# Optimization experiments

Hardware: AMD Instinct MI355X
Metric: run time of the kernel (lower is better)

The kernel has to match this reference:

```python
import jax, jax.numpy as jnp
import numpy as np
import math

A = 32; B = 32; PSIZE = 16; K = 3; STRIDE = 2; PAD = 1; ITERS = 3; FINAL_LAMBDA = 0.01
KK = K * K; KKA = KK * A; KKA2 = KKA // 2 + 1
EPS = 1e-12; LN2PI = math.log(2 * math.pi)


def unfold(x, k, s, p):
    # torch F.unfold: output feature dim ordered (C, kh, kw), columns row-major
    b, C, h, w = x.shape
    xp = jnp.pad(x, ((0, 0), (0, 0), (p, p), (p, p)))
    oh = (h + 2 * p - k) // s + 1
    ow = (w + 2 * p - k) // s + 1
    cols = [xp[:, :, ki:ki + s * (oh - 1) + 1:s, kj:kj + s * (ow - 1) + 1:s]
            for ki in range(k) for kj in range(k)]
    patches = jnp.stack(cols, axis=2)  # [b, C, kk, oh, ow]
    return patches.reshape(b, C, k * k, oh * ow), oh, ow


def setup_inputs():
    key = jax.random.key(0)
    ks = jax.random.split(key, 8)
    b, h, w = 4, 14, 14
    a_in = jax.random.uniform(ks[0], (b, A, h, w), dtype=jnp.float32)
    pose = jax.random.normal(ks[1], (b, A * PSIZE, h, w), dtype=jnp.float32)
    mpose_w = jax.random.normal(ks[2], (B * PSIZE, PSIZE), dtype=jnp.float32) / np.float32(np.sqrt(PSIZE))
    mpose_b = jnp.zeros((B * PSIZE,), jnp.float32)
    freq_w = jax.random.normal(ks[3], (KKA2, PSIZE, 2), dtype=jnp.float32) * 0.02
    ln_g = jnp.ones((A,), jnp.float32)
    ln_b = jnp.zeros((A,), jnp.float32)
    lim = np.float32(np.sqrt(6.0 / (KK + KK)))  # xavier_uniform on [kk, kk, 1]
    spat_w = jax.random.uniform(ks[4], (KK, KK, 1), jnp.float32, -lim, lim)
    spat_bias = jnp.ones((KK,), jnp.float32)
    beta_u = jnp.zeros((1, 1, B, 1), jnp.float32)
    beta_a = jnp.zeros((1, 1, B), jnp.float32)
    return dict(a_in=a_in, pose=pose, mpose_w=mpose_w, mpose_b=mpose_b,
                freq_w=freq_w, ln_g=ln_g, ln_b=ln_b, spat_w=spat_w,
                spat_bias=spat_bias, beta_u=beta_u, beta_a=beta_a)


def _forward(a_in, pose, mpose_w, mpose_b, freq_w, ln_g, ln_b,
             spat_w, spat_bias, beta_u, beta_a):
    b = a_in.shape[0]
    pose_u, oh, ow = unfold(pose, K, STRIDE, PAD)  # [b, A*PSIZE, KK, l]
    l = oh * ow
    pose_u = pose_u.reshape(b, A, PSIZE, KK, l)
    pose_u = pose_u.transpose(0, 4, 3, 1, 2).reshape(b, l, KKA, PSIZE)
    # mpose linear: psize -> B*psize
    po = jnp.einsum('blkp,qp->blkq', pose_u, mpose_w) + mpose_b
    po = po.reshape(b * l, KKA, B, PSIZE)
    # Frequency FFT filter over kkA axis (weight shared across all B slices)
    xf = jnp.fft.rfft(po, axis=1, norm='ortho')        # [bl, KKA2, B, PSIZE] complex
    wc = freq_w[..., 0] + 1j * freq_w[..., 1]           # [KKA2, PSIZE]
    xf = xf * wc[None, :, None, :]
    po = jnp.fft.irfft(xf, n=KKA, axis=1, norm='ortho') + po  # residual
    v = po.reshape(b, l, KKA, B, PSIZE)
    a_u, _, _ = unfold(a_in, K, STRIDE, PAD)            # [b, A, KK, l]
    a_u = a_u.transpose(0, 3, 2, 1).reshape(b, l, KKA)
    # Spatial gating applied to ones-initialized r (identical for every B slice)
    ones = jnp.ones((b * l, KKA), jnp.float32)
    g = ones.reshape(b * l, KK, A)
    mu_g = g.mean(-1, keepdims=True)
    var_g = ((g - mu_g) ** 2).mean(-1, keepdims=True)
    gn = (g - mu_g) / jnp.sqrt(var_g + 1e-5) * ln_g + ln_b
    g2 = jnp.einsum('ij,nja->nia', spat_w[:, :, 0], gn) + spat_bias[None, :, None]
    gate = jax.nn.gelu(g2, approximate=False).reshape(b * l, KKA) + ones
    logit = jnp.broadcast_to(gate[:, :, None], (b * l, KKA, B))
    r = jax.nn.softmax(logit, axis=2).reshape(b, l, KKA, B, 1)
    a_out = mu = None
    for i in range(ITERS):
        lam = FINAL_LAMBDA * (1.0 - 0.95 ** (i + 1))
        # m-step
        rr = r * a_u[:, :, :, None, None]
        r_sum = rr.sum(axis=2, keepdims=True)                 # [b,l,1,B,1]
        coeff = rr / (r_sum + EPS)
        mu = (coeff * v).sum(axis=2, keepdims=True)           # [b,l,1,B,PSIZE]
        sig = (coeff * (v - mu) ** 2).sum(axis=2, keepdims=True) + EPS
        cost = (beta_u + jnp.log(jnp.sqrt(sig[:, :, 0]))) * r_sum[:, :, 0]  # [b,l,B,PSIZE]
        a_out = jax.nn.sigmoid(lam * (beta_a - cost.sum(axis=3)))           # [b,l,B]
        if i < ITERS - 1:
            # e-step (note: log(sigma_sq * ln2pi) is faithful to the original code)
            ln_p = (-0.5 * jnp.sum(jnp.log(sig * LN2PI), axis=-1)
                    - jnp.sum((v - mu) ** 2 / (2.0 * sig), axis=-1))        # [b,l,KKA,B]
            ln_ap = ln_p + jnp.log(a_out[:, :, None, :])
            r = jax.nn.softmax(ln_ap, axis=-1)[..., None]
    pose_out = mu[:, :, 0].reshape(b, l, B * PSIZE).transpose(0, 2, 1).reshape(b, B * PSIZE, oh, ow)
    a_fin = a_out.transpose(0, 2, 1).reshape(b, B, oh, ow)
    return a_fin, pose_out


def reference(a_in, pose, mpose_w, mpose_b, freq_w, ln_g, ln_b,
              spat_w, spat_bias, beta_u, beta_a):
    return _forward(a_in, pose, mpose_w, mpose_b, freq_w, ln_g, ln_b,
                    spat_w, spat_bias, beta_u, beta_a)
```

## Files before the change

kernel.cpp:

```cpp
#include <hip/hip_runtime.h>
#include <hip/hip_bf16.h>
#include <math.h>

#define A_    32
#define B_    32
#define PS    16
#define KK_   9
#define KKA_  288
#define OH_   7
#define L_    49
#define NB    4
#define NSITE 196

#define LAM1 5.0e-4f
#define LAM2 9.75e-4f
#define LAM3 1.42625e-3f
#define LOG_LN2PI 0.6086775903077413f

typedef _Float16 half2v __attribute__((ext_vector_type(2)));
typedef _Float16 half4v __attribute__((ext_vector_type(4)));
typedef short    short8 __attribute__((ext_vector_type(8)));
typedef float    floatx4 __attribute__((ext_vector_type(4)));

#if defined(__has_attribute)
#  if __has_attribute(amdgpu_num_vgpr)
#    define KEM_VGPR_ATTR __attribute__((amdgpu_num_vgpr(224)))
#  else
#    define KEM_VGPR_ATTR
#  endif
#else
#  define KEM_VGPR_ATTR
#endif

static __device__ __forceinline__ float san(float x, float lo, float hi){
    return fminf(fmaxf(x, lo), hi);
}

static __device__ __forceinline__ float dot2acc(half2v a, half2v b, float c){
#if __has_builtin(__builtin_amdgcn_fdot2)
    return __builtin_amdgcn_fdot2(a, b, c, false);
#else
    return c + (float)a.x*(float)b.x + (float)a.y*(float)b.y;
#endif
}

static __device__ __forceinline__ void sched_fence(){
#if __has_builtin(__builtin_amdgcn_sched_barrier)
    __builtin_amdgcn_sched_barrier(0);
#else
    asm volatile("" ::: "memory");
#endif
}

__global__ void k_prep(const float* __restrict__ fw, const float* __restrict__ pose,
                       ushort* __restrict__ cpr, float* __restrict__ csum,
                       __hip_bfloat16* __restrict__ Xt, int n0, int cols, int nx)
{
    if ((int)blockIdx.x >= nx){
        int id = ((int)blockIdx.x - nx)*256 + threadIdx.x;
        if (id >= 16*288) return;
        int p = id / 288, m = id % 288;
        float acc = fw[(0*16 + p)*2 + 0];
        for (int k = 1; k <= 143; ++k){
            float re = fw[(k*16 + p)*2 + 0];
            float im = fw[(k*16 + p)*2 + 1];
            int km = (k*m) % 288;
            float ang = 0.021816615649929116f * (float)km;
            float s, c; sincosf(ang, &s, &c);
            acc += 2.0f*(re*c - im*s);
        }
        float re144 = fw[(144*16 + p)*2 + 0];
        acc += re144 * ((m & 1) ? -1.0f : 1.0f);
        float cv = acc * (1.0f/288.0f);
        if (m == 0) cv += 1.0f;
        cv = san(cv, -1e4f, 1e4f);

        __hip_bfloat16 hb = __float2bfloat16(cv);
        float hif = __bfloat162float(hb);
        __hip_bfloat16 lb = __float2bfloat16(cv - hif);
        ushort hi = *(ushort*)&hb, lo = *(ushort*)&lb;

        ushort* c0h = cpr + p*592;
        ushort* c1h = cpr + 16*592   + p*592;
        ushort* c0l = cpr + 16*592*2 + p*592;
        ushort* c1l = cpr + 16*592*3 + p*592;
        int x1 = 288 - m;
        c0h[x1] = hi;  c0l[x1] = lo;
        c1h[x1-1] = hi; c1l[x1-1] = lo;
        if (m >= 1){
            int x2 = 576 - m;
            c0h[x2] = hi;  c0l[x2] = lo;
            c1h[x2-1] = hi; c1l[x2-1] = lo;
        } else {
            c0h[0] = hi; c0l[0] = lo;
            csum[p] = san(1.0f + fw[(0*16 + p)*2 + 0], -1e4f, 1e4f);
        }
        return;
    }
    int id = blockIdx.x*256 + threadIdx.x;
    if (id >= cols*KKA_) return;
    int c = id / KKA_, j = id % KKA_;
    int n = n0 + (c >> 4), q = c & 15;
    int bs = n / L_, l = n % L_, oy = l / OH_, ox = l % OH_;
    int kk = j >> 5, a = j & 31;
    int y = oy*2 - 1 + kk/3, x = ox*2 - 1 + kk%3;
    float v = 0.f;
    if ((unsigned)y < 14u && (unsigned)x < 14u)
        v = pose[((bs*(A_*PS) + a*PS + q)*14 + y)*14 + x];
    Xt[id] = __float2bfloat16(san(v, -1e4f, 1e4f));
}

__launch_bounds__(256)
__global__ void k_stageB(const ushort* __restrict__ cpr, const __hip_bfloat16* __restrict__ Xt,
                         _Float16* __restrict__ U, int cols, int ns)
{
    const int bx = blockIdx.x, by = blockIdx.y, p = blockIdx.z;
    const int t = threadIdx.x;
    const int w = t >> 6, lane = t & 63;
    const int mn = lane & 15, quad = lane >> 4;
    const int i0 = by*48;
    const int col = bx*64 + w*16 + mn;
    const int colc = (col < cols) ? col : (cols - 1);

    const ushort* c0h = cpr + p*592;
    const ushort* c1h = cpr + 16*592   + p*592;
    const ushort* c0l = cpr + 16*592*2 + p*592;
    const ushort* c1l = cpr + 16*592*3 + p*592;

    floatx4 acc[3] = {{0,0,0,0},{0,0,0,0},{0,0,0,0}};
    for (int k0 = 0; k0 < 288; k0 += 32){
        short8 bfrag = *(const short8*)&Xt[colc*KKA_ + k0 + quad*8];
        #pragma unroll
        for (int s = 0; s < 3; ++s){
            int o = 288 + k0 + quad*8 - (i0 + s*16 + mn);
            int sel = o & 1;
            int off = o - sel;
            const ushort* bh = sel ? c1h : c0h;
            const ushort* bl = sel ? c1l : c0l;
            short8 ah = *(const short8*)&bh[off];
            short8 al = *(const short8*)&bl[off];
            acc[s] = __builtin_amdgcn_mfma_f32_16x16x32_bf16(ah, bfrag, acc[s], 0, 0, 0);
            acc[s] = __builtin_amdgcn_mfma_f32_16x16x32_bf16(al, bfrag, acc[s], 0, 0, 0);
        }
    }
    if (col < cols){
        const int nn = col >> 4, q0 = col & 15;
        #pragma unroll
        for (int s = 0; s < 3; ++s){
            #pragma unroll
            for (int r = 0; r < 4; ++r){
                int i = i0 + s*16 + quad*4 + r;
                U[(i*ns + nn)*256 + p*16 + q0] = (_Float16)acc[s][r];
            }
        }
    }
}

__launch_bounds__(512, 2) KEM_VGPR_ATTR
__global__ void
k_em(const _Float16* __restrict__ U, const float* __restrict__ a_in,
     const float* __restrict__ mpw, const float* __restrict__ mpb,
     const float* __restrict__ csum,
     const float* __restrict__ beta_u, const float* __restrict__ beta_a,
     int n0, int ns, float* __restrict__ out)
{
    const int nl = blockIdx.x;
    const int n  = n0 + nl;
    const int t = threadIdx.x;
    const int Bc = t >> 4, p = t & 15;
    const int bs = n / L_, l = n % L_;

    __shared__ uint  v_lds[72][512];
    __shared__ float a_s[KKA_];
    __shared__ float d_s[16][33];
    __shared__ float rbuf[16][33];
    __shared__ float cst[32];

    for (int j = t; j < KKA_; j += 512){
        int kk = j >> 5, a = j & 31;
        int oy = l / OH_, ox = l % OH_;
        int y = oy*2 - 1 + kk/3, x = ox*2 - 1 + kk%3;
        float v = 0.f;
        if ((unsigned)y < 14u && (unsigned)x < 14u)
            v = a_in[((bs*A_ + a)*14 + y)*14 + x];
        a_s[j] = san(v, 0.f, 1e4f);
    }
    half2v w_h[8];
    #pragma unroll
    for (int k = 0; k < 8; ++k){
        w_h[k].x = (_Float16)mpw[t*16 + 2*k];
        w_h[k].y = (_Float16)mpw[t*16 + 2*k + 1];
    }
    const float vb = mpb[t] * csum[p];
    const float bu = beta_u[Bc];
    const float ba = beta_a[Bc];
    __syncthreads();

    float S0tot = 0.f;
    for (int j = 0; j < KKA_; ++j) S0tot += a_s[j];

    const _Float16* Up = U + nl*256 + p*16;
    const int istr = ns*256;

    float S1 = 0.f, S2 = 0.f;

    half2v v_h[72];
    #pragma unroll
    for (int g = 0; g < 36; ++g){
        #pragma unroll
        for (int k2 = 0; k2 < 2; ++k2){
            const int pr = g*2 + k2;
            const int i0 = 144 + pr*2;
            union { uint4 u4; half2v h2[4]; } A0, A1, B0, B1;
            A0.u4 = *(const uint4*)&Up[i0*istr];
            A1.u4 = *(const uint4*)&Up[i0*istr + 8];
            B0.u4 = *(const uint4*)&Up[(i0+1)*istr];
            B1.u4 = *(const uint4*)&Up[(i0+1)*istr + 8];
            float v0 = vb, v1 = vb;
            #pragma unroll
            for (int m = 0; m < 4; ++m){
                v0 = dot2acc(A0.h2[m], w_h[m],   v0);
                v0 = dot2acc(A1.h2[m], w_h[4+m], v0);
                v1 = dot2acc(B0.h2[m], w_h[m],   v1);
                v1 = dot2acc(B1.h2[m], w_h[4+m], v1);
            }
            const float a0 = a_s[i0], a1 = a_s[i0+1];
            S1 += a0*v0 + a1*v1;
            S2 += a0*v0*v0 + a1*v1*v1;
            half2v vh; vh.x = (_Float16)v0; vh.y = (_Float16)v1;
            v_h[pr] = vh;
        }
        sched_fence();
    }

    for (int ch = 0; ch < 9; ++ch){
        #pragma unroll
        for (int k = 0; k < 8; ++k){
            const int i0 = ch*16 + 2*k;
            union { uint4 u4; half2v h2[4]; } A0, A1, B0, B1;
            A0.u4 = *(const uint4*)&Up[i0*istr];
            A1.u4 = *(const uint4*)&Up[i0*istr + 8];
            B0.u4 = *(const uint4*)&Up[(i0+1)*istr];
            B1.u4 = *(const uint4*)&Up[(i0+1)*istr + 8];
            float v0 = vb, v1 = vb;
            #pragma unroll
            for (int m = 0; m < 4; ++m){
                v0 = dot2acc(A0.h2[m], w_h[m],   v0);
                v0 = dot2acc(A1.h2[m], w_h[4+m], v0);
                v1 = dot2acc(B0.h2[m], w_h[m],   v1);
                v1 = dot2acc(B1.h2[m], w_h[4+m], v1);
            }
            const float a0 = a_s[i0], a1 = a_s[i0+1];
            S1 += a0*v0 + a1*v1;
            S2 += a0*v0*v0 + a1*v1*v1;
            union { half2v h; uint u; } cv;
            cv.h.x = (_Float16)v0; cv.h.y = (_Float16)v1;
            v_lds[ch*8 + k][t] = cv.u;
        }
    }

    float mu_r, i2s_r;
    {
        const float rs  = S0tot * (1.0f/32.0f);
        const float inv = 1.0f / (rs + 1e-12f);
        const float S1r = S1 * (1.0f/32.0f), S2r = S2 * (1.0f/32.0f);
        mu_r = S1r * inv;
        const float sg  = fmaxf((S2r - 2.f*mu_r*S1r + mu_r*mu_r*rs) * inv, 0.f) + 1e-12f;
        i2s_r = 0.5f / sg;
        const float lg  = logf(sg);
        float cs = (bu + 0.5f*lg) * rs;
        float ls = lg + LOG_LN2PI;
        #pragma unroll
        for (int m = 1; m < 16; m <<= 1){ cs += __shfl_xor(cs, m, 16); ls += __shfl_xor(ls, m, 16); }
        const float aout = san(1.f/(1.f + expf(-LAM1*(ba - cs))), 1e-30f, 1.f);
        if (p == 0) cst[Bc] = logf(aout) - 0.5f*ls;
    }
    __syncthreads();

    const int b0 = p & 1, b1 = (p>>1)&1, b2 = (p>>2)&1, b3 = (p>>3)&1;
    float muF = 0.f, aF = 0.f;
    for (int it = 0; it < 2; ++it){
        const float lam = it ? LAM3 : LAM2;
        float T0 = 0.f, T1 = 0.f, T2 = 0.f;

        auto process = [&](int ibase, auto getpair){
            float e1[8], e2[4], e3[2], dfin;
            #pragma unroll
            for (int s = 0; s < 8; ++s){
                float v0, v1; getpair(s, v0, v1);
                float d0 = v0 - mu_r, d1 = v1 - mu_r;
                float ea = d0*d0*i2s_r, eb = d1*d1*i2s_r;
                float aown  = b0 ? eb : ea;
                float asend = b0 ? ea : eb;
                e1[s] = aown + __shfl_xor(asend, 1);
            }
            #pragma unroll
            for (int s = 0; s < 4; ++s){
                float aown  = b1 ? e1[2*s+1] : e1[2*s];
                float asend = b1 ? e1[2*s]   : e1[2*s+1];
                e2[s] = aown + __shfl_xor(asend, 2);
            }
            #pragma unroll
            for (int s = 0; s < 2; ++s){
                float aown  = b2 ? e2[2*s+1] : e2[2*s];
                float asend = b2 ? e2[2*s]   : e2[2*s+1];
                e3[s] = aown + __shfl_xor(asend, 4);
            }
            {
                float aown  = b3 ? e3[1] : e3[0];
                float asend = b3 ? e3[0] : e3[1];
                dfin = aown + __shfl_xor(asend, 8);
            }
            d_s[p][Bc] = dfin;
            __syncthreads();
            {
                const int isub = t >> 5, Bce = t & 31;
                float lnap = cst[Bce] - d_s[isub][Bce];
                float mx = lnap;
                #pragma unroll
                for (int m = 16; m >= 1; m >>= 1) mx = fmaxf(mx, __shfl_xor(mx, m));
                float ex = expf(lnap - mx);
                float sm = ex;
                #pragma unroll
                for (int m = 16; m >= 1; m >>= 1) sm += __shfl_xor(sm, m);
                rbuf[isub][Bce] = (ex / sm) * a_s[ibase + isub];
            }
            __syncthreads();
            #pragma unroll
            for (int s = 0; s < 8; ++s){
                float v0, v1; getpair(s, v0, v1);
                float r0 = rbuf[2*s][Bc], r1 = rbuf[2*s+1][Bc];
                T0 += r0 + r1;
                T1 += r0*v0 + r1*v1;
                T2 += r0*v0*v0 + r1*v1*v1;
            }
        };

        for (int ch = 0; ch < 9; ++ch){
            process(ch*16, [&](int s, float& v0, float& v1){
                union { uint u; half2v h; } cv; cv.u = v_lds[ch*8 + s][t];
                v0 = (float)cv.h.x; v1 = (float)cv.h.y;
            });
        }
        #pragma unroll
        for (int ch = 0; ch < 9; ++ch){
            process(144 + ch*16, [&](int s, float& v0, float& v1){
                half2v vh = v_h[ch*8 + s];
                v0 = (float)vh.x; v1 = (float)vh.y;
            });
        }

        const float inv = 1.f/(T0 + 1e-12f);
        const float mu  = T1 * inv;
        const float sg  = fmaxf((T2 - 2.f*mu*T1 + mu*mu*T0) * inv, 0.f) + 1e-12f;
        const float lg  = logf(sg);
        float cs = (bu + 0.5f*lg) * T0;
        float ls = lg + LOG_LN2PI;
        #pragma unroll
        for (int m = 1; m < 16; m <<= 1){ cs += __shfl_xor(cs, m, 16); ls += __shfl_xor(ls, m, 16); }
        const float aout = san(1.f/(1.f + expf(-lam*(ba - cs))), 1e-30f, 1.f);
        if (it == 0){
            mu_r = mu; i2s_r = 0.5f/sg;
            if (p == 0) cst[Bc] = logf(aout) - 0.5f*ls;
            __syncthreads();
        } else { muF = mu; aF = aout; }
    }

    if (p == 0) out[bs*(B_*L_) + Bc*L_ + l] = san(aF, 0.f, 1.f);
    out[6272 + (bs*512 + t)*L_ + l] = san(muF, -1e4f, 1e4f);
}

extern "C" void kernel_launch(void* const* d_in, const int* in_sizes, int n_in,
                              void* d_out, int out_size, void* d_ws, size_t ws_size,
                              hipStream_t stream)
{
    const float* a_in   = (const float*)d_in[0];
    const float* pose   = (const float*)d_in[1];
    const float* mpw    = (const float*)d_in[2];
    const float* mpb    = (const float*)d_in[3];
    const float* fw     = (const float*)d_in[4];
    const float* beta_u = (const float*)d_in[9];
    const float* beta_a = (const float*)d_in[10];
    float* out = (float*)d_out;

    char* base = (char*)d_ws;
    float*  csum = (float*)(base + 0);
    ushort* cpr  = (ushort*)(base + 256);

    const int opts[] = {196, 98, 49, 28, 14, 7, 4, 2, 1};
    int ns = 1;
    for (int oi = 0; oi < 9; ++oi){
        size_t need = 76288u + (size_t)156672u * (size_t)opts[oi];
        if (need <= ws_size){ ns = opts[oi]; break; }
    }
    const int G = NSITE / ns;
    const int cols = ns * PS;
    __hip_bfloat16* Xt = (__hip_bfloat16*)(base + 76288);
    _Float16*       Ug = (_Float16*)(base + 76288 + (size_t)9216*ns);

    for (int g = 0; g < G; ++g){
        const int n0 = g * ns;
        const int nx = (cols*KKA_ + 255)/256;
        const int nc = (g == 0) ? 18 : 0;
        k_prep  <<<nx + nc, 256, 0, stream>>>(fw, pose, cpr, csum, Xt, n0, cols, nx);
        k_stageB<<<dim3((cols + 63)/64, 6, 16), 256, 0, stream>>>(cpr, Xt, Ug, cols, ns);
        k_em    <<<ns, 512, 0, stream>>>(Ug, a_in, mpw, mpb, csum, beta_u, beta_a, n0, ns, out);
    }
}
```

Before: 281.1 us.

## Batch three E-step chunks per barrier pair and reorder prep blocks

The E-step loop in k_em now handles 48 input capsules (three 16-row groups) between each pair of __syncthreads, instead of 16, which cuts barrier count threefold. The separate rbuf array is merged into an enlarged d_s buffer that holds the responsibilities in place. k_prep now schedules the coefficient-table blocks first so the long sincos loops start early, and uses the fast __sincosf intrinsic. The cost is more registers and LDS per step, plus slightly lower sincos accuracy.

Measured after the change: 258.2 us. 1.09x faster.

```diff
diff --git a/kernel.cpp b/kernel.cpp
--- a/kernel.cpp
+++ b/kernel.cpp
@@ -54,10 +54,10 @@
 
 __global__ void k_prep(const float* __restrict__ fw, const float* __restrict__ pose,
                        ushort* __restrict__ cpr, float* __restrict__ csum,
-                       __hip_bfloat16* __restrict__ Xt, int n0, int cols, int nx)
+                       __hip_bfloat16* __restrict__ Xt, int n0, int cols, int nc)
 {
-    if ((int)blockIdx.x >= nx){
-        int id = ((int)blockIdx.x - nx)*256 + threadIdx.x;
+    if ((int)blockIdx.x < nc){
+        int id = (int)blockIdx.x*256 + threadIdx.x;
         if (id >= 16*288) return;
         int p = id / 288, m = id % 288;
         float acc = fw[(0*16 + p)*2 + 0];
@@ -66,7 +66,7 @@
             float im = fw[(k*16 + p)*2 + 1];
             int km = (k*m) % 288;
             float ang = 0.021816615649929116f * (float)km;
-            float s, c; sincosf(ang, &s, &c);
+            float s, c; __sincosf(ang, &s, &c);
             acc += 2.0f*(re*c - im*s);
         }
         float re144 = fw[(144*16 + p)*2 + 0];
@@ -97,7 +97,7 @@
         }
         return;
     }
-    int id = blockIdx.x*256 + threadIdx.x;
+    int id = ((int)blockIdx.x - nc)*256 + threadIdx.x;
     if (id >= cols*KKA_) return;
     int c = id / KKA_, j = id % KKA_;
     int n = n0 + (c >> 4), q = c & 15;
@@ -171,9 +171,8 @@
     const int bs = n / L_, l = n % L_;
 
     __shared__ uint  v_lds[72][512];
+    __shared__ float d_s[48][33];
     __shared__ float a_s[KKA_];
-    __shared__ float d_s[16][33];
-    __shared__ float rbuf[16][33];
     __shared__ float cst[32];
 
     for (int j = t; j < KKA_; j += 512){
@@ -283,73 +282,82 @@
         const float lam = it ? LAM3 : LAM2;
         float T0 = 0.f, T1 = 0.f, T2 = 0.f;
 
-        auto process = [&](int ibase, auto getpair){
-            float e1[8], e2[4], e3[2], dfin;
+        #pragma unroll
+        for (int ch = 0; ch < 6; ++ch){
             #pragma unroll
-            for (int s = 0; s < 8; ++s){
-                float v0, v1; getpair(s, v0, v1);
-                float d0 = v0 - mu_r, d1 = v1 - mu_r;
-                float ea = d0*d0*i2s_r, eb = d1*d1*i2s_r;
-                float aown  = b0 ? eb : ea;
-                float asend = b0 ? ea : eb;
-                e1[s] = aown + __shfl_xor(asend, 1);
-            }
-            #pragma unroll
-            for (int s = 0; s < 4; ++s){
-                float aown  = b1 ? e1[2*s+1] : e1[2*s];
-                float asend = b1 ? e1[2*s]   : e1[2*s+1];
-                e2[s] = aown + __shfl_xor(asend, 2);
-            }
-            #pragma unroll
-            for (int s = 0; s < 2; ++s){
-                float aown  = b2 ? e2[2*s+1] : e2[2*s];
-                float asend = b2 ? e2[2*s]   : e2[2*s+1];
-                e3[s] = aown + __shfl_xor(asend, 4);
-            }
-            {
-                float aown  = b3 ? e3[1] : e3[0];
-                float asend = b3 ? e3[0] : e3[1];
-                dfin = aown + __shfl_xor(asend, 8);
-            }
-            d_s[p][Bc] = dfin;
+            for (int g = 0; g < 3; ++g){
+                float e1[8], e2[4], e3[2], dfin;
+                #pragma unroll
+                for (int s = 0; s < 8; ++s){
+                    const int pr = ch*24 + g*8 + s;
+                    float v0, v1;
+                    if (ch < 3){
+                        union { uint u; half2v h; } cv; cv.u = v_lds[pr][t];
+                        v0 = (float)cv.h.x; v1 = (float)cv.h.y;
+                    } else {
+                        half2v vh = v_h[pr - 72];
+                        v0 = (float)vh.x; v1 = (float)vh.y;
+                    }
+                    float d0 = v0 - mu_r, d1 = v1 - mu_r;
+                    float ea = d0*d0*i2s_r, eb = d1*d1*i2s_r;
+                    float aown  = b0 ? eb : ea;
+                    float asend = b0 ? ea : eb;
+                    e1[s] = aown + __shfl_xor(asend, 1);
+                }
+                #pragma unroll
+                for (int s = 0; s < 4; ++s){
+                    float aown  = b1 ? e1[2*s+1] : e1[2*s];
+                    float asend = b1 ? e1[2*s]   : e1[2*s+1];
+                    e2[s] = aown + __shfl_xor(asend, 2);
+                }
+                #pragma unroll
+                for (int s = 0; s < 2; ++s){
+                    float aown  = b2 ? e2[2*s+1] : e2[2*s];
+                    float asend = b2 ? e2[2*s]   : e2[2*s+1];
+                    e3[s] = aown + __shfl_xor(asend, 4);
+                }
+                {
+                    float aown  = b3 ? e3[1] : e3[0];
+                    float asend = b3 ? e3[0] : e3[1];
+                    dfin = aown + __shfl_xor(asend, 8);
+                }
+                d_s[g*16 + p][Bc] = dfin;
+            }
             __syncthreads();
             {
                 const int isub = t >> 5, Bce = t & 31;
-                float lnap = cst[Bce] - d_s[isub][Bce];
-                float mx = lnap;
                 #pragma unroll
-                for (int m = 16; m >= 1; m >>= 1) mx = fmaxf(mx, __shfl_xor(mx, m));
-                float ex = expf(lnap - mx);
-                float sm = ex;
-                #pragma unroll
-                for (int m = 16; m >= 1; m >>= 1) sm += __shfl_xor(sm, m);
-                rbuf[isub][Bce] = (ex / sm) * a_s[ibase + isub];
+                for (int rr = 0; rr < 3; ++rr){
+                    const int row = rr*16 + isub;
+                    float lnap = cst[Bce] - d_s[row][Bce];
+                    float mx = lnap;
+                    #pragma unroll
+                    for (int m = 16; m >= 1; m >>= 1) mx = fmaxf(mx, __shfl_xor(mx, m));
+                    float ex = expf(lnap - mx);
+                    float sm = ex;
+                    #pragma unroll
+                    for (int m = 16; m >= 1; m >>= 1) sm += __shfl_xor(sm, m);
+                    d_s[row][Bce] = (ex / sm) * a_s[ch*48 + row];
+                }
             }
             __syncthreads();
             #pragma unroll
-            for (int s = 0; s < 8; ++s){
-                float v0, v1; getpair(s, v0, v1);
-                float r0 = rbuf[2*s][Bc], r1 = rbuf[2*s+1][Bc];
+            for (int s = 0; s < 24; ++s){
+                const int pr = ch*24 + s;
+                float v0, v1;
+                if (ch < 3){
+                    union { uint u; half2v h; } cv; cv.u = v_lds[pr][t];
+                    v0 = (float)cv.h.x; v1 = (float)cv.h.y;
+                } else {
+                    half2v vh = v_h[pr - 72];
+                    v0 = (float)vh.x; v1 = (float)vh.y;
+                }
+                float r0 = d_s[2*s][Bc], r1 = d_s[2*s+1][Bc];
                 T0 += r0 + r1;
                 T1 += r0*v0 + r1*v1;
                 T2 += r0*v0*v0 + r1*v1*v1;
             }
-        };
-
-        for (int ch = 0; ch < 9; ++ch){
-            process(ch*16, [&](int s, float& v0, float& v1){
-                union { uint u; half2v h; } cv; cv.u = v_lds[ch*8 + s][t];
-                v0 = (float)cv.h.x; v1 = (float)cv.h.y;
-            });
-        }
-        #pragma unroll
-        for (int ch = 0; ch < 9; ++ch){
-            process(144 + ch*16, [&](int s, float& v0, float& v1){
-                half2v vh = v_h[ch*8 + s];
-                v0 = (float)vh.x; v1 = (float)vh.y;
-            });
-        }
-
+        }
         const float inv = 1.f/(T0 + 1e-12f);
         const float mu  = T1 * inv;
         const float sg  = fmaxf((T2 - 2.f*mu*T1 + mu*mu*T0) * inv, 0.f) + 1e-12f;
@@ -402,7 +410,7 @@
         const int n0 = g * ns;
         const int nx = (cols*KKA_ + 255)/256;
         const int nc = (g == 0) ? 18 : 0;
-        k_prep  <<<nx + nc, 256, 0, stream>>>(fw, pose, cpr, csum, Xt, n0, cols, nx);
+        k_prep  <<<nx + nc, 256, 0, stream>>>(fw, pose, cpr, csum, Xt, n0, cols, nc);
         k_stageB<<<dim3((cols + 63)/64, 6, 16), 256, 0, stream>>>(cpr, Xt, Ug, cols, ns);
         k_em    <<<ns, 512, 0, stream>>>(Ug, a_in, mpw, mpb, csum, beta_u, beta_a, n0, ns, out);
     }
```
